# Optimization experiments

Measured on AMD Instinct MI355X. Metric: run time of the kernel, lower is better.

The kernel has to match this reference:

```python
import jax, jax.numpy as jnp
import numpy as np

NHID = 512
NCLS = 250
CHUNK = 200  # words per class (equal class_chunks), vocab = NCLS*CHUNK = 50000
N = 2048     # flattened tokens (batch*seq after masking)


def setup_inputs() -> dict:
    key = jax.random.key(0)
    k1, k2, k3, k4, k5 = jax.random.split(key, 5)
    r = 0.1  # init_weights uniform range
    x = jax.random.normal(k1, (N, NHID), dtype=jnp.float32)
    cls_idx = jax.random.randint(k2, (N,), 0, NCLS, dtype=jnp.int64)
    Wc = jax.random.uniform(k3, (NCLS, NHID), jnp.float32, -r, r)   # cls_decoder.weight
    bc = jnp.zeros((NCLS,), jnp.float32)                             # cls_decoder.bias
    Ww = jax.random.uniform(k4, (NCLS, CHUNK, NHID), jnp.float32, -r, r)  # stacked words_decoders weights
    bw = jnp.zeros((NCLS, CHUNK), jnp.float32)                       # stacked words_decoders biases
    return {"x": x, "Wc": Wc, "bc": bc, "Ww": Ww, "bw": bw, "cls_idx": cls_idx}


def reference(x, Wc, bc, Ww, bw, cls_idx):
    # Class logits for every token: cls_decoder(input)
    p_class = jnp.einsum('nh,ch->nc', x, Wc) + bc          # [N, NCLS]
    # Per-class word decoders: each token goes through the Linear of its class.
    # Equivalent to the dict-based index_select + per-class Linear in the
    # original forward (rows reordered per-token instead of grouped by class).
    Wg = Ww[cls_idx]                                       # [N, CHUNK, NHID] irregular gather
    bg = bw[cls_idx]                                       # [N, CHUNK]
    p_words = jnp.einsum('nkh,nh->nk', Wg, x) + bg         # [N, CHUNK]
    # Concatenate class and within-class logits into one array output.
    return jnp.concatenate([p_class, p_words], axis=1)     # [N, NCLS+CHUNK]
```

## Files before the change

### kernel.cpp

```cpp
#include <hip/hip_runtime.h>

#define NHID   512
#define NCLS   250
#define CHUNK  200
#define NTOK   2048
#define NOUT   450
#define NPAN   13
#define NWB    (NCLS * NPAN)
#define NCB    256
#define NBLK   (NWB + NCB)
#define NTHR   64
#define MAXTOK 64

typedef __attribute__((ext_vector_type(8))) short bf16x8;
typedef __attribute__((ext_vector_type(4))) float f32x4;

#define MFMA(a, b, c) __builtin_amdgcn_mfma_f32_16x16x32_bf16((a), (b), (c), 0, 0, 0)

__device__ __forceinline__ unsigned hpack(unsigned a, unsigned b) {
    return __builtin_amdgcn_perm(a, b, 0x07060302u);
}

__device__ __forceinline__ void cvt8(float4 va, float4 vb, bf16x8& h, bf16x8& l) {
    unsigned u0 = __float_as_uint(va.x), u1 = __float_as_uint(va.y);
    unsigned u2 = __float_as_uint(va.z), u3 = __float_as_uint(va.w);
    unsigned u4 = __float_as_uint(vb.x), u5 = __float_as_uint(vb.y);
    unsigned u6 = __float_as_uint(vb.z), u7 = __float_as_uint(vb.w);
    union { unsigned w[4]; bf16x8 v; } H, L;
    H.w[0] = hpack(u1, u0); H.w[1] = hpack(u3, u2);
    H.w[2] = hpack(u5, u4); H.w[3] = hpack(u7, u6);
    float r0 = va.x - __uint_as_float(u0 & 0xffff0000u);
    float r1 = va.y - __uint_as_float(u1 & 0xffff0000u);
    float r2 = va.z - __uint_as_float(u2 & 0xffff0000u);
    float r3 = va.w - __uint_as_float(u3 & 0xffff0000u);
    float r4 = vb.x - __uint_as_float(u4 & 0xffff0000u);
    float r5 = vb.y - __uint_as_float(u5 & 0xffff0000u);
    float r6 = vb.z - __uint_as_float(u6 & 0xffff0000u);
    float r7 = vb.w - __uint_as_float(u7 & 0xffff0000u);
    L.w[0] = hpack(__float_as_uint(r1), __float_as_uint(r0));
    L.w[1] = hpack(__float_as_uint(r3), __float_as_uint(r2));
    L.w[2] = hpack(__float_as_uint(r5), __float_as_uint(r4));
    L.w[3] = hpack(__float_as_uint(r7), __float_as_uint(r6));
    h = H.v; l = L.v;
}

__device__ __forceinline__ void lds_fence_wave() {
    __builtin_amdgcn_wave_barrier();
    asm volatile("s_waitcnt lgkmcnt(0)" ::: "memory");
    __builtin_amdgcn_wave_barrier();
}

__global__ __launch_bounds__(NTHR, 3)
void cbd_fused(const float* __restrict__ x,  const float* __restrict__ Wc,
               const float* __restrict__ bc, const float* __restrict__ Ww,
               const float* __restrict__ bw, const int* __restrict__ cls_idx,
               float* __restrict__ out)
{
    const int bid  = blockIdx.x;
    const int lane = threadIdx.x;
    const int n    = lane & 15;
    const int q    = lane >> 4;

    if (bid < NCB) {
        const int mt = bid >> 1, hn = bid & 1;
        const float* ap = x + (size_t)(mt * 16 + n) * NHID + q * 8;
        #pragma unroll
        for (int g4 = 0; g4 < 2; ++g4) {
            const float* bp[4]; float bias[4]; int col[4]; bool rv[4];
            #pragma unroll
            for (int k = 0; k < 4; ++k) {
                int r = (hn * 8 + g4 * 4 + k) * 16 + n;
                rv[k] = r < NCLS;
                int rc = rv[k] ? r : NCLS - 1;
                bp[k]   = Wc + (size_t)rc * NHID + q * 8;
                bias[k] = bc[rc];
                col[k]  = rc;
            }
            f32x4 acc[4] = {{0,0,0,0},{0,0,0,0},{0,0,0,0},{0,0,0,0}};
            float4 qa[2][2], qb[2][8];
            #pragma unroll
            for (int j = 0; j < 2; ++j) {
                qa[j][0] = *(const float4*)(ap + j * 32);
                qa[j][1] = *(const float4*)(ap + j * 32 + 4);
                #pragma unroll
                for (int k = 0; k < 4; ++k) {
                    qb[j][2*k]   = *(const float4*)(bp[k] + j * 32);
                    qb[j][2*k+1] = *(const float4*)(bp[k] + j * 32 + 4);
                }
            }
            #pragma unroll 2
            for (int s = 0; s < 16; ++s) {
                const int b = s & 1;
                bf16x8 ah, al; cvt8(qa[b][0], qa[b][1], ah, al);
                #pragma unroll
                for (int k = 0; k < 4; ++k) {
                    bf16x8 bh, bl; cvt8(qb[b][2*k], qb[b][2*k+1], bh, bl);
                    acc[k] = MFMA(ah, bh, acc[k]);
                    acc[k] = MFMA(al, bh, acc[k]);
                    acc[k] = MFMA(ah, bl, acc[k]);
                }
                if (s + 2 < 16) {
                    qa[b][0] = *(const float4*)(ap + (s+2) * 32);
                    qa[b][1] = *(const float4*)(ap + (s+2) * 32 + 4);
                    #pragma unroll
                    for (int k = 0; k < 4; ++k) {
                        qb[b][2*k]   = *(const float4*)(bp[k] + (s+2) * 32);
                        qb[b][2*k+1] = *(const float4*)(bp[k] + (s+2) * 32 + 4);
                    }
                }
            }
            #pragma unroll
            for (int k = 0; k < 4; ++k)
                if (rv[k]) {
                    #pragma unroll
                    for (int i = 0; i < 4; ++i)
                        out[(size_t)(mt * 16 + q * 4 + i) * NOUT + col[k]]
                            = acc[k][i] + bias[k];
                }
        }
        return;
    }

    const int wb = bid - NCB;
    const int c = wb / NPAN;
    const int p = wb - c * NPAN;

    const int r  = p * 16 + n;
    const int rr = r < CHUNK ? r : CHUNK - 1;
    const float* wp = Ww + ((size_t)c * CHUNK + rr) * NHID + q * 8;

    float4 pb[2][4];
    #pragma unroll
    for (int j = 0; j < 2; ++j)
        #pragma unroll
        for (int t = 0; t < 2; ++t) {
            pb[j][2*t]   = *(const float4*)(wp + (2*j + t) * 32);
            pb[j][2*t+1] = *(const float4*)(wp + (2*j + t) * 32 + 4);
        }

    int myvals[32];
    #pragma unroll
    for (int it = 0; it < 8; ++it) {
        int4 v = *(const int4*)&cls_idx[it * 256 + lane * 4];
        myvals[it*4+0] = v.x; myvals[it*4+1] = v.y;
        myvals[it*4+2] = v.z; myvals[it*4+3] = v.w;
    }
    __shared__ int toktmp[MAXTOK];
    int cnt = 0;
    #pragma unroll
    for (int j = 0; j < 32; ++j) {
        int idx  = (j >> 2) * 256 + lane * 4 + (j & 3);
        bool hit = (myvals[j] == c);
        unsigned long long m = __ballot(hit);
        if (hit) {
            int pos = cnt + (int)__popcll(m & ((1ull << lane) - 1ull));
            if (pos < MAXTOK) toktmp[pos] = idx;
        }
        cnt += (int)__popcll(m);
    }
    if (cnt == 0) return;
    const int cntc = cnt < MAXTOK ? cnt : MAXTOK;
    lds_fence_wave();

    const float bias = bw[c * CHUNK + rr];

    for (int sb = 0; sb < cntc; sb += 16) {
        int slot  = sb + n;
        int mytok = toktmp[slot < cntc ? slot : 0];
        int tkS[4]; bool msk[4];
        #pragma unroll
        for (int i = 0; i < 4; ++i) {
            int m = q * 4 + i;
            tkS[i] = __shfl(mytok, m);
            msk[i] = (sb + m) < cntc;
        }
        const float* apx = x + (size_t)mytok * NHID + q * 8;

        float4 pa[2][4];
        #pragma unroll
        for (int j = 0; j < 2; ++j)
            #pragma unroll
            for (int t = 0; t < 2; ++t) {
                pa[j][2*t]   = *(const float4*)(apx + (2*j + t) * 32);
                pa[j][2*t+1] = *(const float4*)(apx + (2*j + t) * 32 + 4);
            }
        if (sb > 0) {
            #pragma unroll
            for (int j = 0; j < 2; ++j)
                #pragma unroll
                for (int t = 0; t < 2; ++t) {
                    pb[j][2*t]   = *(const float4*)(wp + (2*j + t) * 32);
                    pb[j][2*t+1] = *(const float4*)(wp + (2*j + t) * 32 + 4);
                }
        }

        f32x4 acc = {0.f, 0.f, 0.f, 0.f};
        #pragma unroll 2
        for (int j = 0; j < 8; ++j) {
            const int b = j & 1;
            #pragma unroll
            for (int t = 0; t < 2; ++t) {
                bf16x8 ah, al, bh, bl;
                cvt8(pa[b][2*t], pa[b][2*t+1], ah, al);
                cvt8(pb[b][2*t], pb[b][2*t+1], bh, bl);
                acc = MFMA(ah, bh, acc);
                acc = MFMA(al, bh, acc);
                acc = MFMA(ah, bl, acc);
            }
            if (j + 2 < 8) {
                #pragma unroll
                for (int t = 0; t < 2; ++t) {
                    const int s = 2 * (j + 2) + t;
                    pa[b][2*t]   = *(const float4*)(apx + s * 32);
                    pa[b][2*t+1] = *(const float4*)(apx + s * 32 + 4);
                    pb[b][2*t]   = *(const float4*)(wp + s * 32);
                    pb[b][2*t+1] = *(const float4*)(wp + s * 32 + 4);
                }
            }
        }

        if (r < CHUNK) {
            #pragma unroll
            for (int i = 0; i < 4; ++i)
                if (msk[i])
                    out[(size_t)tkS[i] * NOUT + NCLS + r] = acc[i] + bias;
        }
    }
}

extern "C" void kernel_launch(void* const* d_in, const int* in_sizes, int n_in,
                              void* d_out, int out_size, void* d_ws, size_t ws_size,
                              hipStream_t stream) {
    const float* x   = (const float*)d_in[0];
    const float* Wc  = (const float*)d_in[1];
    const float* bc  = (const float*)d_in[2];
    const float* Ww  = (const float*)d_in[3];
    const float* bw  = (const float*)d_in[4];
    const int*   cls = (const int*)d_in[5];
    float* out = (float*)d_out;
    hipLaunchKernelGGL(cbd_fused, dim3(NBLK), dim3(NTHR), 0, stream,
                       x, Wc, bc, Ww, bw, cls, out);
}
```

Measured before the change: 174.4 us.

## Stage word-decoder weight panel into LDS via async global_load_lds with swizzle

Each word block now copies its 16x512 weight panel into a 32KB LDS buffer using async global-to-LDS loads with an XOR swizzle, issued before the class-index scan so the copy overlaps it. The MFMA loop then reads B operands from LDS instead of re-fetching them from global memory for every 16-token sub-batch. The inner loop is fully unrolled and launch_bounds no longer requests 3 blocks per CU. The cost is higher LDS use per block, which may cut occupancy, plus hand-placed vmcnt waits that must match the number of outstanding loads.

```diff
diff --git a/kernel.cpp b/kernel.cpp
--- a/kernel.cpp
+++ b/kernel.cpp
@@ -16,6 +16,8 @@
 typedef __attribute__((ext_vector_type(4))) float f32x4;
 
 #define MFMA(a, b, c) __builtin_amdgcn_mfma_f32_16x16x32_bf16((a), (b), (c), 0, 0, 0)
+
+#define BOFF(s) ((((s) >> 3) * 256) + (((s) & 7) * 32))
 
 __device__ __forceinline__ unsigned hpack(unsigned a, unsigned b) {
     return __builtin_amdgcn_perm(a, b, 0x07060302u);
@@ -44,18 +46,27 @@
     h = H.v; l = L.v;
 }
 
+__device__ __forceinline__ void async16(const float* g, float* lds_base) {
+    __builtin_amdgcn_global_load_lds(
+        (const __attribute__((address_space(1))) unsigned*)g,
+        (__attribute__((address_space(3))) unsigned*)lds_base, 16, 0, 0);
+}
+
 __device__ __forceinline__ void lds_fence_wave() {
     __builtin_amdgcn_wave_barrier();
     asm volatile("s_waitcnt lgkmcnt(0)" ::: "memory");
     __builtin_amdgcn_wave_barrier();
 }
 
-__global__ __launch_bounds__(NTHR, 3)
+__global__ __launch_bounds__(NTHR)
 void cbd_fused(const float* __restrict__ x,  const float* __restrict__ Wc,
                const float* __restrict__ bc, const float* __restrict__ Ww,
                const float* __restrict__ bw, const int* __restrict__ cls_idx,
                float* __restrict__ out)
 {
+    __shared__ float Bbuf[16 * 512];
+    __shared__ int   toktmp[MAXTOK];
+
     const int bid  = blockIdx.x;
     const int lane = threadIdx.x;
     const int n    = lane & 15;
@@ -127,16 +138,6 @@
 
     const int r  = p * 16 + n;
     const int rr = r < CHUNK ? r : CHUNK - 1;
-    const float* wp = Ww + ((size_t)c * CHUNK + rr) * NHID + q * 8;
-
-    float4 pb[2][4];
-    #pragma unroll
-    for (int j = 0; j < 2; ++j)
-        #pragma unroll
-        for (int t = 0; t < 2; ++t) {
-            pb[j][2*t]   = *(const float4*)(wp + (2*j + t) * 32);
-            pb[j][2*t+1] = *(const float4*)(wp + (2*j + t) * 32 + 4);
-        }
 
     int myvals[32];
     #pragma unroll
@@ -145,7 +146,22 @@
         myvals[it*4+0] = v.x; myvals[it*4+1] = v.y;
         myvals[it*4+2] = v.z; myvals[it*4+3] = v.w;
     }
-    __shared__ int toktmp[MAXTOK];
+    float bias = bw[c * CHUNK + rr];
+    #pragma unroll
+    for (int it = 0; it < 8; ++it)
+        asm volatile("" :: "v"(myvals[it*4]), "v"(myvals[it*4+1]),
+                           "v"(myvals[it*4+2]), "v"(myvals[it*4+3]));
+    asm volatile("" :: "v"(bias));
+
+    #pragma unroll
+    for (int j = 0; j < 16; ++j) {
+        int rj = p * 16 + j; if (rj > CHUNK - 1) rj = CHUNK - 1;
+        const float* srow = Ww + ((size_t)c * CHUNK + rj) * NHID;
+        const int lsw = (lane ^ (j & 7)) << 2;
+        async16(srow + lsw,       &Bbuf[j * 512]);
+        async16(srow + 256 + lsw, &Bbuf[j * 512 + 256]);
+    }
+
     int cnt = 0;
     #pragma unroll
     for (int j = 0; j < 32; ++j) {
@@ -158,11 +174,15 @@
         }
         cnt += (int)__popcll(m);
     }
-    if (cnt == 0) return;
+    if (cnt == 0) {
+        asm volatile("s_waitcnt vmcnt(0)" ::: "memory");
+        return;
+    }
     const int cntc = cnt < MAXTOK ? cnt : MAXTOK;
     lds_fence_wave();
 
-    const float bias = bw[c * CHUNK + rr];
+    const float* Bb0 = Bbuf + n * 512 + (((q * 8))     ^ ((n & 7) << 2));
+    const float* Bb1 = Bbuf + n * 512 + (((q * 8) + 4) ^ ((n & 7) << 2));
 
     for (int sb = 0; sb < cntc; sb += 16) {
         int slot  = sb + n;
@@ -184,25 +204,20 @@
                 pa[j][2*t]   = *(const float4*)(apx + (2*j + t) * 32);
                 pa[j][2*t+1] = *(const float4*)(apx + (2*j + t) * 32 + 4);
             }
-        if (sb > 0) {
-            #pragma unroll
-            for (int j = 0; j < 2; ++j)
-                #pragma unroll
-                for (int t = 0; t < 2; ++t) {
-                    pb[j][2*t]   = *(const float4*)(wp + (2*j + t) * 32);
-                    pb[j][2*t+1] = *(const float4*)(wp + (2*j + t) * 32 + 4);
-                }
-        }
+        asm volatile("s_waitcnt vmcnt(8)" ::: "memory");
 
         f32x4 acc = {0.f, 0.f, 0.f, 0.f};
-        #pragma unroll 2
+        #pragma unroll
         for (int j = 0; j < 8; ++j) {
             const int b = j & 1;
             #pragma unroll
             for (int t = 0; t < 2; ++t) {
+                const int s = 2 * j + t;
                 bf16x8 ah, al, bh, bl;
                 cvt8(pa[b][2*t], pa[b][2*t+1], ah, al);
-                cvt8(pb[b][2*t], pb[b][2*t+1], bh, bl);
+                float4 b0 = *(const float4*)(Bb0 + BOFF(s));
+                float4 b1 = *(const float4*)(Bb1 + BOFF(s));
+                cvt8(b0, b1, bh, bl);
                 acc = MFMA(ah, bh, acc);
                 acc = MFMA(al, bh, acc);
                 acc = MFMA(ah, bl, acc);
@@ -213,8 +228,6 @@
                     const int s = 2 * (j + 2) + t;
                     pa[b][2*t]   = *(const float4*)(apx + s * 32);
                     pa[b][2*t+1] = *(const float4*)(apx + s * 32 + 4);
-                    pb[b][2*t]   = *(const float4*)(wp + s * 32);
-                    pb[b][2*t+1] = *(const float4*)(wp + s * 32 + 4);
                 }
             }
         }
```

Measured after the change: 177.9 us. Within noise of the previous version (+2.0%).
